# Performance work log

Measured on AMD Instinct MI355X. Metric: run time of the kernel, lower is better.

## Reference

```python
import jax, jax.numpy as jnp
import numpy as np


def setup_inputs() -> dict:
    key = jax.random.key(0)
    ks = jax.random.split(key, 7)
    b, t, c = 2, 2048, 1024
    s = 0.02  # keep pre-softmax logits in a sane range
    return {
        "query": jax.random.normal(ks[0], (b, t, c), jnp.float32),
        "key": jax.random.normal(ks[1], (b, t, c), jnp.float32),
        "value": jax.random.normal(ks[2], (b, t, c), jnp.float32),
        "in_proj_w": jax.random.normal(ks[3], (3 * c, c), jnp.float32) * s,
        "in_proj_b": jax.random.normal(ks[4], (3 * c,), jnp.float32) * s,
        "out_proj_w": jax.random.normal(ks[5], (c, c), jnp.float32) * s,
        "out_proj_b": jax.random.normal(ks[6], (c,), jnp.float32) * s,
        "window_size": 128,
    }


def reference(query, key, value, in_proj_w, in_proj_b, out_proj_w, out_proj_b, window_size):
    num_heads = 16
    b, t, c = query.shape
    hd = c // num_heads
    wq, wk, wv = in_proj_w[:c], in_proj_w[c:2 * c], in_proj_w[2 * c:]
    bq, bk, bv = in_proj_b[:c], in_proj_b[c:2 * c], in_proj_b[2 * c:]
    # project and split heads: [b, h, t, hd]
    q = (query @ wq.T + bq).reshape(b, t, num_heads, hd).transpose(0, 2, 1, 3)
    k = (key @ wk.T + bk).reshape(b, t, num_heads, hd).transpose(0, 2, 1, 3)
    v = (value @ wv.T + bv).reshape(b, t, num_heads, hd).transpose(0, 2, 1, 3)
    # NOTE: torch adds a *float* attn_mask to the logits. The original mask is
    # 1.0 inside the sliding window, 0.0 outside -- an additive +1 bias, NOT -inf.
    idx = jnp.arange(t)
    band = (jnp.abs(idx[:, None] - idx[None, :]) <= window_size).astype(q.dtype)  # [t, t]
    scale = 1.0 / jnp.sqrt(jnp.asarray(hd, q.dtype))
    logits = jnp.einsum("bhqd,bhkd->bhqk", q * scale, k) + band  # [b,h,t,t]
    attn = jax.nn.softmax(logits, axis=-1)
    out = jnp.einsum("bhqk,bhkd->bhqd", attn, v)  # [b,h,t,hd]
    out = out.transpose(0, 2, 1, 3).reshape(b, t, c)
    return out @ out_proj_w.T + out_proj_b
```

## Files before the change

### kernel.cpp

```cpp
#include <hip/hip_runtime.h>

typedef __attribute__((ext_vector_type(8)))  short short8;
typedef __attribute__((ext_vector_type(4)))  float f32x4;
typedef __attribute__((ext_vector_type(16))) float f32x16;
typedef __attribute__((ext_vector_type(2)))  unsigned uint2v;

constexpr int B  = 2;
constexpr int T  = 2048;
constexpr int C  = 1024;
constexpr int H  = 16;
constexpr int HD = 64;

__device__ inline unsigned bf16rne(float a){
  unsigned u = __builtin_bit_cast(unsigned, a);
  u += 0x7fffu + ((u >> 16) & 1u);
  return u >> 16;
}
__device__ inline unsigned bf16pair(float a, float b){
  unsigned ua = __builtin_bit_cast(unsigned, a); ua += 0x7fffu + ((ua >> 16) & 1u);
  unsigned ub = __builtin_bit_cast(unsigned, b); ub += 0x7fffu + ((ub >> 16) & 1u);
  return (ua >> 16) | (ub & 0xffff0000u);
}
__device__ inline void gll16(const void* g, void* l){
  __builtin_amdgcn_global_load_lds(
      (const __attribute__((address_space(1))) unsigned*)g,
      (__attribute__((address_space(3))) unsigned*)l, 16, 0, 0);
}
__device__ inline float exp2f_(float x){
#if __has_builtin(__builtin_amdgcn_exp2f)
  return __builtin_amdgcn_exp2f(x);
#else
  return __builtin_exp2f(x);
#endif
}

__global__ void convert_w(const float* __restrict__ ipw, const float* __restrict__ opw,
                          unsigned* __restrict__ dst)
{
  const int i = blockIdx.x * 256 + threadIdx.x;
  const long e = (long)i * 8;
  const float* src; long off;
  if (e < 3145728) { src = ipw; off = e; }
  else             { src = opw; off = e - 3145728; }
  const float4 x0 = *(const float4*)(src + off);
  const float4 x1 = *(const float4*)(src + off + 4);
  uint4 st;
  st.x = bf16pair(x0.x, x0.y); st.y = bf16pair(x0.z, x0.w);
  st.z = bf16pair(x1.x, x1.y); st.w = bf16pair(x1.z, x1.w);
  *(uint4*)(dst + (size_t)i*4) = st;
}

__global__ __launch_bounds__(256, 5) void gemm_qkv(
    const float* __restrict__ A0, const float* __restrict__ A1,
    const float* __restrict__ A2,
    const unsigned short* __restrict__ Wb, const float* __restrict__ bias,
    unsigned short* __restrict__ Qb, unsigned short* __restrict__ Kf,
    unsigned short* __restrict__ Vf)
{
  __shared__ __align__(16) char gsm[24576];
  unsigned short* As = (unsigned short*)gsm;
  unsigned short* Bs = (unsigned short*)(gsm + 8192);

  const int tid  = threadIdx.x, lane = tid & 63, wn = tid >> 6;
  const int bm   = blockIdx.x, bn = blockIdx.y;
  const int m16  = lane & 15, quad = lane >> 4;

  const int which = bn >> 3;
  const float* A = (which == 0) ? A0 : (which == 1 ? A1 : A2);

  f32x4 acc[4][2];
#pragma unroll
  for (int i = 0; i < 4; i++)
#pragma unroll
    for (int j = 0; j < 2; j++) acc[i][j] = (f32x4){0.f, 0.f, 0.f, 0.f};

  const int srowA = wn * 16 + (lane >> 3);
  const int srowW = wn * 32 + (lane >> 3);
  const int skp   = (((lane & 7) ^ (lane >> 3))) * 8;
  const int xr    = m16 & 7;

  const float* ap[2];
#pragma unroll
  for (int p = 0; p < 2; p++)
    ap[p] = A + (size_t)(bm*64 + srowA + p*8)*1024 + skp;

  float4 ar0[2], ar1[2];
#pragma unroll
  for (int p = 0; p < 2; p++) {
    ar0[p] = *(const float4*)(ap[p]);
    ar1[p] = *(const float4*)(ap[p] + 4);
  }

  for (int k0 = 0; k0 < 1024; k0 += 64) {
    __syncthreads();
#pragma unroll
    for (int p = 0; p < 4; p++)
      gll16(Wb + (size_t)(bn*128 + srowW + p*8)*1024 + k0 + skp, (char*)Bs + wn*4096 + p*1024);
#pragma unroll
    for (int p = 0; p < 2; p++) {
      uint4 st;
      st.x = bf16pair(ar0[p].x, ar0[p].y); st.y = bf16pair(ar0[p].z, ar0[p].w);
      st.z = bf16pair(ar1[p].x, ar1[p].y); st.w = bf16pair(ar1[p].z, ar1[p].w);
      *(uint4*)((char*)As + wn*2048 + p*1024 + lane*16) = st;
    }
    __syncthreads();

    const int k0n = (k0 + 64 < 1024) ? k0 + 64 : 0;
#pragma unroll
    for (int p = 0; p < 2; p++) {
      ar0[p] = *(const float4*)(ap[p] + k0n);
      ar1[p] = *(const float4*)(ap[p] + k0n + 4);
    }

#pragma unroll
    for (int kk = 0; kk < 2; kk++) {
      const int ch = ((kk*4 + quad) ^ xr) * 16;
      short8 af[4], bf[2];
#pragma unroll
      for (int i = 0; i < 4; i++)
        af[i] = *(const short8*)((const char*)As + (i*16 + m16)*128 + ch);
#pragma unroll
      for (int j = 0; j < 2; j++)
        bf[j] = *(const short8*)((const char*)Bs + (wn*32 + j*16 + m16)*128 + ch);
#pragma unroll
      for (int i = 0; i < 4; i++)
#pragma unroll
        for (int j = 0; j < 2; j++)
          acc[i][j] = __builtin_amdgcn_mfma_f32_16x16x32_bf16(af[i], bf[j], acc[i][j], 0,0,0);
    }
  }

  __syncthreads();
  float* Ls = (float*)gsm;
  const int hbase = (bn & 7) * 2;
  const int b  = bm >> 5;
  const int tbase = (bm & 31) * 64;
  const int kt = bm & 31;
  const float ksc = (which == 1) ? 0.18033688f : 1.0f;

  if (which < 2) {
#pragma unroll
    for (int j = 0; j < 2; ++j) {
      const float bj = bias[bn*128 + wn*32 + j*16 + m16] * ksc;
#pragma unroll
      for (int i = 0; i < 4; ++i) {
        const int m0 = i*16 + quad*4;
#pragma unroll
        for (int r = 0; r < 4; ++r)
          Ls[(m0 + r)*67 + wn*16 + m16] = __builtin_fmaf(acc[i][j][r], ksc, bj);
      }
      __syncthreads();
#pragma unroll
      for (int r2 = 0; r2 < 2; ++r2) {
        const int v = r2*256 + tid;
        const int m = v & 63, seg = v >> 6;
        const float* src = &Ls[m*67 + seg*8];
        const float4 f0 = *(const float4*)src;
        const float4 f1 = *(const float4*)(src + 4);
        uint4 st;
        st.x = bf16pair(f0.x, f0.y); st.y = bf16pair(f0.z, f0.w);
        st.z = bf16pair(f1.x, f1.y); st.w = bf16pair(f1.z, f1.w);
        const int gcol = (seg >> 1)*32 + j*16 + (seg & 1)*8;
        const int bhh  = b*16 + hbase + (gcol >> 6);
        const int d0   = gcol & 63;
        if (which == 0) {
          *(uint4*)&Qb[((size_t)(bhh*2048) + tbase + m)*64 + d0] = st;
        } else {
          const int wkk = (m >> 5) & 1, ln2 = m & 31;
          const int s = d0 >> 4, h2 = (d0 >> 3) & 1;
          uint4* dp = (uint4*)Kf + ((size_t)(bhh*32 + kt)*8 + s*2 + wkk)*64 + h2*32 + ln2;
          *dp = st;
        }
      }
      __syncthreads();
    }
  } else {
#pragma unroll
    for (int j = 0; j < 2; ++j) {
      const float bj = bias[bn*128 + wn*32 + j*16 + m16];
      const int cc = wn*16 + m16;
#pragma unroll
      for (int i = 0; i < 4; ++i) {
        f32x4 tv = acc[i][j];
        tv[0] += bj; tv[1] += bj; tv[2] += bj; tv[3] += bj;
        *(f32x4*)&Ls[cc*68 + i*16 + quad*4] = tv;
      }
      __syncthreads();
#pragma unroll
      for (int r2 = 0; r2 < 2; ++r2) {
        const int v = r2*256 + tid;
        const int n = v >> 3, mseg = v & 7;
        const float* src = &Ls[n*68 + mseg*8];
        const float4 f0 = *(const float4*)src;
        const float4 f1 = *(const float4*)(src + 4);
        uint4 st;
        st.x = bf16pair(f0.x, f0.y); st.y = bf16pair(f0.z, f0.w);
        st.z = bf16pair(f1.x, f1.y); st.w = bf16pair(f1.z, f1.w);
        const int gcol = (n >> 4)*32 + j*16 + (n & 15);
        const int d    = gcol & 63;
        const int bhh  = b*16 + hbase + (gcol >> 6);
        const int wkk = mseg >> 2, cc2 = (mseg >> 1) & 1, h2 = mseg & 1;
        const int dt = d >> 5, ln2 = d & 31;
        uint4* dp = (uint4*)Vf + (size_t)(bhh*32 + kt)*512 + dt*256 + cc2*128 + wkk*64 + h2*32 + ln2;
        *dp = st;
      }
      __syncthreads();
    }
  }
}

__global__ __launch_bounds__(256, 4) void gemm_out(
    const unsigned short* __restrict__ Ab, const unsigned short* __restrict__ Wb,
    const float* __restrict__ bias, float* __restrict__ outF)
{
  __shared__ __align__(16) char gsm[16384];
  unsigned short* As = (unsigned short*)gsm;
  unsigned short* Ws = (unsigned short*)(gsm + 8192);

  const int tid  = threadIdx.x, lane = tid & 63, wv = tid >> 6;
  const int bm   = blockIdx.x, bn = blockIdx.y;
  const int m16  = lane & 15, quad = lane >> 4;

  f32x4 acc[4];
#pragma unroll
  for (int i = 0; i < 4; i++) acc[i] = (f32x4){0.f, 0.f, 0.f, 0.f};

  const int srow = wv * 16 + (lane >> 3);
  const int skp  = (((lane & 7) ^ (lane >> 3))) * 8;
  const int xr   = m16 & 7;

  for (int k0 = 0; k0 < 1024; k0 += 64) {
    __syncthreads();
#pragma unroll
    for (int p = 0; p < 2; p++) {
      gll16(Ab + (size_t)(bm*64 + srow + p*8)*1024 + k0 + skp, (char*)As + wv*2048 + p*1024);
      gll16(Wb + (size_t)(bn*64 + srow + p*8)*1024 + k0 + skp, (char*)Ws + wv*2048 + p*1024);
    }
    __syncthreads();

#pragma unroll
    for (int kk = 0; kk < 2; kk++) {
      const int ch = ((kk*4 + quad) ^ xr) * 16;
      short8 af[4], bf;
#pragma unroll
      for (int i = 0; i < 4; i++)
        af[i] = *(const short8*)((const char*)As + (i*16 + m16)*128 + ch);
      bf = *(const short8*)((const char*)Ws + (wv*16 + m16)*128 + ch);
#pragma unroll
      for (int i = 0; i < 4; i++)
        acc[i] = __builtin_amdgcn_mfma_f32_16x16x32_bf16(af[i], bf, acc[i], 0,0,0);
    }
  }

  const int n_e = bn*64 + wv*16 + m16;
  const float bj = bias[n_e];
#pragma unroll
  for (int i = 0; i < 4; i++) {
    const int mbase = bm*64 + i*16 + quad*4;
#pragma unroll
    for (int r = 0; r < 4; r++)
      outF[(size_t)(mbase + r) * 1024 + n_e] = acc[i][r] + bj;
  }
}

__global__ __launch_bounds__(256, 3) void attn_k(
    const unsigned short* __restrict__ Qb, const unsigned short* __restrict__ Kf,
    const unsigned short* __restrict__ Vf, const int* __restrict__ wptr,
    unsigned short* __restrict__ ctx)
{
  __shared__ __align__(16) char smem[16896];
  float* Om   = (float*)smem;
  float* lbuf = (float*)(smem + 16384);

  const int tid = threadIdx.x, lane = tid & 63, wv = tid >> 6;
  const int wq = wv >> 1, wk = wv & 1;
  const int h = lane >> 5, ln = lane & 31;
  const int bh = blockIdx.x, qt = blockIdx.y;
  const int win = *wptr;
  const int q0 = qt * 64 + wq * 32;
  const size_t hb = (size_t)bh * T * HD;

  constexpr float LOG2E = 1.44269504f;

  short8 qf[4];
#pragma unroll
  for (int s = 0; s < 4; s++)
    qf[s] = *(const short8*)(Qb + hb + (size_t)(q0 + ln)*64 + s*16 + h*8);

  short8 onesv;
#pragma unroll
  for (int jj = 0; jj < 8; jj++) onesv[jj] = (short)0x3F80;

  f32x16 O0, O1, Lacc, Zv;
#pragma unroll
  for (int r = 0; r < 16; r++) { O0[r] = 0.f; O1[r] = 0.f; Lacc[r] = 0.f; Zv[r] = 0.f; }
  const int tq = q0 + ln;

  const uint4* kbase = (const uint4*)Kf + (size_t)bh*32*512 + wk*64 + lane;
  const uint4* vbase = (const uint4*)Vf + (size_t)bh*32*512 + wk*64 + lane;

  uint4 kA[4], vA[4];
#pragma unroll
  for (int s = 0; s < 4; s++) kA[s] = kbase[s*128];
#pragma unroll
  for (int u = 0; u < 4; u++) vA[u] = vbase[(u >> 1)*256 + (u & 1)*128];

  for (int kt = 0; kt < 32; ++kt) {
    f32x16 st;
#pragma unroll
    for (int s = 0; s < 4; s++) {
      const short8 kf2 = __builtin_bit_cast(short8, kA[s]);
      st = __builtin_amdgcn_mfma_f32_32x32x16_bf16(kf2, qf[s], (s == 0 ? Zv : st), 0, 0, 0);
    }
    if (kt < 31) {
      const size_t o = (size_t)(kt + 1) * 512;
#pragma unroll
      for (int s = 0; s < 4; s++) kA[s] = kbase[o + s*128];
    }

    const int kb = kt*64 + wk*32;
    int sep = 0;
    if (kb > q0 + 31) sep = kb - (q0 + 31);
    else if (q0 > kb + 31) sep = q0 - (kb + 31);
    const int d1 = kb + 31 - q0, d2 = q0 + 31 - kb;
    const int dmax = max(d1 < 0 ? -d1 : d1, d2 < 0 ? -d2 : d2);

    float pr[16];
    if (sep > win) {
#pragma unroll
      for (int r = 0; r < 16; r++) pr[r] = exp2f_(st[r]);
    } else if (dmax <= win) {
#pragma unroll
      for (int r = 0; r < 16; r++) pr[r] = exp2f_(st[r] + LOG2E);
    } else {
      const int tkb = kb + 4*h;
#pragma unroll
      for (int r = 0; r < 16; r++) {
        const int tk = tkb + (r & 3) + 8*(r >> 2);
        int dd = tq - tk; dd = dd < 0 ? -dd : dd;
        pr[r] = exp2f_(st[r] + (dd <= win ? LOG2E : 0.0f));
      }
    }

    unsigned pk[8];
#pragma unroll
    for (int g = 0; g < 8; g++)
      pk[g] = __builtin_amdgcn_perm(__builtin_bit_cast(unsigned, pr[2*g+1]),
                                    __builtin_bit_cast(unsigned, pr[2*g]),
                                    0x07060302u);

#pragma unroll
    for (int c = 0; c < 2; c++) {
      const uint2v s02 = __builtin_amdgcn_permlane32_swap(pk[4*c+0], pk[4*c+2], false, false);
      const uint2v s13 = __builtin_amdgcn_permlane32_swap(pk[4*c+1], pk[4*c+3], false, false);
      union { unsigned u[4]; short8 v; } P;
      P.u[0] = s02[0];
      P.u[1] = s13[0];
      P.u[2] = s02[1];
      P.u[3] = s13[1];
#pragma unroll
      for (int dt = 0; dt < 2; dt++) {
        const short8 vf2 = __builtin_bit_cast(short8, vA[dt*2 + c]);
        if (dt == 0) O0 = __builtin_amdgcn_mfma_f32_32x32x16_bf16(P.v, vf2, O0, 0,0,0);
        else         O1 = __builtin_amdgcn_mfma_f32_32x32x16_bf16(P.v, vf2, O1, 0,0,0);
      }
      Lacc = __builtin_amdgcn_mfma_f32_32x32x16_bf16(P.v, onesv, Lacc, 0,0,0);
    }

    if (kt < 31) {
      const size_t o = (size_t)(kt + 1) * 512;
#pragma unroll
      for (int u = 0; u < 4; u++) vA[u] = vbase[o + (u >> 1)*256 + (u & 1)*128];
    }
  }

  __syncthreads();
  if (wk == 1) {
#pragma unroll
    for (int r = 0; r < 16; r++) {
      Om[wq*2048 + r*64 + lane]        = O0[r];
      Om[wq*2048 + (16 + r)*64 + lane] = O1[r];
    }
    if (ln == 0) {
#pragma unroll
      for (int r = 0; r < 16; r++)
        lbuf[wq*32 + (r & 3) + 8*(r >> 2) + 4*h] = Lacc[r];
    }
  }
  __syncthreads();
  if (wk == 0) {
    const int b = bh >> 4, hh = bh & 15;
#pragma unroll
    for (int r = 0; r < 16; r++) {
      const int qrow = (r & 3) + 8*(r >> 2) + 4*h;
      const float lt = Lacc[r] + lbuf[wq*32 + qrow];
      const float linv = 1.0f / lt;
      const int t = q0 + qrow;
      const float o0 = (O0[r] + Om[wq*2048 + r*64 + lane]) * linv;
      const float o1 = (O1[r] + Om[wq*2048 + (16 + r)*64 + lane]) * linv;
      unsigned short* cp = ctx + (size_t)(b*2048 + t)*1024 + hh*64;
      cp[ln]      = (unsigned short)bf16rne(o0);
      cp[32 + ln] = (unsigned short)bf16rne(o1);
    }
  }
}

extern "C" void kernel_launch(void* const* d_in, const int* in_sizes, int n_in,
                              void* d_out, int out_size, void* d_ws, size_t ws_size,
                              hipStream_t stream)
{
  const float* query = (const float*)d_in[0];
  const float* key   = (const float*)d_in[1];
  const float* value = (const float*)d_in[2];
  const float* ipw   = (const float*)d_in[3];
  const float* ipb   = (const float*)d_in[4];
  const float* opw   = (const float*)d_in[5];
  const float* opb   = (const float*)d_in[6];
  const int*   win   = (const int*)d_in[7];

  char* ws = (char*)d_ws;
  unsigned short* Winbf  = (unsigned short*)(ws);
  unsigned short* Woutbf = (unsigned short*)(ws + 6291456);
  unsigned short* Qb     = (unsigned short*)(ws + 33554432);
  unsigned short* Kf     = (unsigned short*)(ws + 41943040);
  unsigned short* Vf     = (unsigned short*)(ws + 50331648);
  unsigned short* ctx    = (unsigned short*)(ws + 58720256);

  convert_w<<<2048, 256, 0, stream>>>(ipw, opw, (unsigned*)ws);

  gemm_qkv<<<dim3(64, 24), 256, 0, stream>>>(
      query, key, value, Winbf, ipb, Qb, Kf, Vf);

  attn_k<<<dim3(32, 32), 256, 0, stream>>>(Qb, Kf, Vf, win, ctx);

  gemm_out<<<dim3(64, 16), 256, 0, stream>>>(
      ctx, Woutbf, opb, (float*)d_out);
}
```

Measured before the change: 213.5 us.

## Double-buffer LDS tiles in QKV projection GEMM to overlap loads with MFMA

```diff
diff --git a/kernel.cpp b/kernel.cpp
--- a/kernel.cpp
+++ b/kernel.cpp
@@ -50,16 +50,16 @@
   *(uint4*)(dst + (size_t)i*4) = st;
 }
 
-__global__ __launch_bounds__(256, 5) void gemm_qkv(
+__global__ __launch_bounds__(256, 3) void gemm_qkv(
     const float* __restrict__ A0, const float* __restrict__ A1,
     const float* __restrict__ A2,
     const unsigned short* __restrict__ Wb, const float* __restrict__ bias,
     unsigned short* __restrict__ Qb, unsigned short* __restrict__ Kf,
     unsigned short* __restrict__ Vf)
 {
-  __shared__ __align__(16) char gsm[24576];
+  __shared__ __align__(16) char gsm[49152];
   unsigned short* As = (unsigned short*)gsm;
-  unsigned short* Bs = (unsigned short*)(gsm + 8192);
+  unsigned short* Bs = (unsigned short*)(gsm + 16384);
 
   const int tid  = threadIdx.x, lane = tid & 63, wn = tid >> 6;
   const int bm   = blockIdx.x, bn = blockIdx.y;
@@ -85,32 +85,55 @@
     ap[p] = A + (size_t)(bm*64 + srowA + p*8)*1024 + skp;
 
   float4 ar0[2], ar1[2];
+
 #pragma unroll
   for (int p = 0; p < 2; p++) {
     ar0[p] = *(const float4*)(ap[p]);
     ar1[p] = *(const float4*)(ap[p] + 4);
   }
+#pragma unroll
+  for (int p = 0; p < 4; p++)
+    gll16(Wb + (size_t)(bn*128 + srowW + p*8)*1024 + skp, (char*)Bs + wn*4096 + p*1024);
+#pragma unroll
+  for (int p = 0; p < 2; p++) {
+    uint4 st;
+    st.x = bf16pair(ar0[p].x, ar0[p].y); st.y = bf16pair(ar0[p].z, ar0[p].w);
+    st.z = bf16pair(ar1[p].x, ar1[p].y); st.w = bf16pair(ar1[p].z, ar1[p].w);
+    *(uint4*)((char*)As + wn*2048 + p*1024 + lane*16) = st;
+  }
+  __syncthreads();
+#pragma unroll
+  for (int p = 0; p < 2; p++) {
+    ar0[p] = *(const float4*)(ap[p] + 64);
+    ar1[p] = *(const float4*)(ap[p] + 68);
+  }
 
   for (int k0 = 0; k0 < 1024; k0 += 64) {
-    __syncthreads();
-#pragma unroll
-    for (int p = 0; p < 4; p++)
-      gll16(Wb + (size_t)(bn*128 + srowW + p*8)*1024 + k0 + skp, (char*)Bs + wn*4096 + p*1024);
-#pragma unroll
-    for (int p = 0; p < 2; p++) {
-      uint4 st;
-      st.x = bf16pair(ar0[p].x, ar0[p].y); st.y = bf16pair(ar0[p].z, ar0[p].w);
-      st.z = bf16pair(ar1[p].x, ar1[p].y); st.w = bf16pair(ar1[p].z, ar1[p].w);
-      *(uint4*)((char*)As + wn*2048 + p*1024 + lane*16) = st;
-    }
-    __syncthreads();
-
-    const int k0n = (k0 + 64 < 1024) ? k0 + 64 : 0;
-#pragma unroll
-    for (int p = 0; p < 2; p++) {
-      ar0[p] = *(const float4*)(ap[p] + k0n);
-      ar1[p] = *(const float4*)(ap[p] + k0n + 4);
-    }
+    const int cur = (k0 >> 6) & 1, nxt = cur ^ 1;
+    if (k0 < 960) {
+#pragma unroll
+      for (int p = 0; p < 2; p++) {
+        uint4 st;
+        st.x = bf16pair(ar0[p].x, ar0[p].y); st.y = bf16pair(ar0[p].z, ar0[p].w);
+        st.z = bf16pair(ar1[p].x, ar1[p].y); st.w = bf16pair(ar1[p].z, ar1[p].w);
+        *(uint4*)((char*)As + nxt*8192 + wn*2048 + p*1024 + lane*16) = st;
+      }
+#pragma unroll
+      for (int p = 0; p < 4; p++)
+        gll16(Wb + (size_t)(bn*128 + srowW + p*8)*1024 + (k0 + 64) + skp,
+              (char*)Bs + nxt*16384 + wn*4096 + p*1024);
+      if (k0 < 896) {
+        const int k0n = k0 + 128;
+#pragma unroll
+        for (int p = 0; p < 2; p++) {
+          ar0[p] = *(const float4*)(ap[p] + k0n);
+          ar1[p] = *(const float4*)(ap[p] + k0n + 4);
+        }
+      }
+    } else {
+      asm volatile("s_waitcnt vmcnt(0)" ::: "memory");
+    }
+    __builtin_amdgcn_sched_barrier(0);
 
 #pragma unroll
     for (int kk = 0; kk < 2; kk++) {
@@ -118,16 +141,19 @@
       short8 af[4], bf[2];
 #pragma unroll
       for (int i = 0; i < 4; i++)
-        af[i] = *(const short8*)((const char*)As + (i*16 + m16)*128 + ch);
+        af[i] = *(const short8*)((const char*)As + cur*8192 + (i*16 + m16)*128 + ch);
 #pragma unroll
       for (int j = 0; j < 2; j++)
-        bf[j] = *(const short8*)((const char*)Bs + (wn*32 + j*16 + m16)*128 + ch);
+        bf[j] = *(const short8*)((const char*)Bs + cur*16384 + (wn*32 + j*16 + m16)*128 + ch);
 #pragma unroll
       for (int i = 0; i < 4; i++)
 #pragma unroll
         for (int j = 0; j < 2; j++)
           acc[i][j] = __builtin_amdgcn_mfma_f32_16x16x32_bf16(af[i], bf[j], acc[i][j], 0,0,0);
     }
+    asm volatile("s_waitcnt lgkmcnt(0)" ::: "memory");
+    __builtin_amdgcn_s_barrier();
+    __builtin_amdgcn_sched_barrier(0);
   }
 
   __syncthreads();
```

Measured after the change: 218.3 us. 2.3% more time.
